# Kernel optimization log

Measured on AMD Instinct MI355X. Metric: run time of the kernel, lower is better.

The kernel has to match this reference:

```python
import jax, jax.numpy as jnp
import numpy as np

N_NODES = 8192
K = 64


def setup_inputs() -> dict:
    key = jax.random.key(0)
    k1, k2 = jax.random.split(key)
    A = jax.random.normal(k1, (N_NODES, N_NODES), dtype=jnp.float32)
    idx = jax.random.randint(k2, (N_NODES,), 0, N_NODES, dtype=jnp.int64)
    return {"A": A, "idx": idx}


def reference(A, idx):
    # adj = relu(A)
    adj = jax.nn.relu(A)
    # per-row top-k indices (dim=1), then scatter a 0/1 mask and multiply
    _, ind = jax.lax.top_k(adj, K)  # ind: [N, K]
    rows = jnp.arange(adj.shape[0], dtype=ind.dtype)[:, None]  # [N, 1]
    mask = jnp.zeros_like(adj).at[rows, ind].set(1.0)
    return adj * mask
```

## Files before the change

kernel.cpp:

```cpp
#include <hip/hip_runtime.h>
#include <stdint.h>


constexpr int N     = 8192;
constexpr int K     = 64;
constexpr int BLOCK = 256;
constexpr int VPT   = N / BLOCK;
constexpr int V4    = VPT / 4;
constexpr int EQ_CAP = 256;

__global__ __launch_bounds__(BLOCK) void topk_row_kernel(
    const float* __restrict__ A, float* __restrict__ out)
{
    __shared__ uint32_t hist[4][256];
    __shared__ uint32_t s_prefix;
    __shared__ uint32_t s_k;
    __shared__ uint32_t s_cnt;
    __shared__ int      s_tzero;
    __shared__ uint32_t s_eq[EQ_CAP];

    const int tid  = threadIdx.x;
    const int wave = tid >> 6;
    const int lane = tid & 63;
    const int row  = blockIdx.x;

    const float4* rowp = reinterpret_cast<const float4*>(A + (size_t)row * N);
    float4*       outp = reinterpret_cast<float4*>(out + (size_t)row * N);

    uint32_t v[VPT];
    #pragma unroll
    for (int j = 0; j < V4; ++j) {
        float4 f = rowp[tid + j * BLOCK];
        v[4*j+0] = (f.x > 0.f) ? __float_as_uint(f.x) : 0u;
        v[4*j+1] = (f.y > 0.f) ? __float_as_uint(f.y) : 0u;
        v[4*j+2] = (f.z > 0.f) ? __float_as_uint(f.z) : 0u;
        v[4*j+3] = (f.w > 0.f) ? __float_as_uint(f.w) : 0u;
    }

    #pragma unroll
    for (int j = 0; j < 4; ++j) hist[j][tid] = 0;
    if (tid == 0) { s_prefix = 0; s_k = K; s_cnt = 0; s_tzero = 0; }
    __syncthreads();

    #pragma unroll
    for (int j = 0; j < VPT; ++j) {
        uint32_t x = v[j];
        if (x) atomicAdd(&hist[wave][x >> 24], 1u);
    }
    __syncthreads();
    {
        uint32_t tot = hist[0][tid] + hist[1][tid] + hist[2][tid] + hist[3][tid];
        hist[0][tid] = tot;
    }
    __syncthreads();

    if (wave == 0) {
        uint32_t k  = s_k;
        uint32_t h0 = hist[0][4*lane+0];
        uint32_t h1 = hist[0][4*lane+1];
        uint32_t h2 = hist[0][4*lane+2];
        uint32_t h3 = hist[0][4*lane+3];
        uint32_t suf = h0 + h1 + h2 + h3;
        #pragma unroll
        for (int d = 1; d < 64; d <<= 1) {
            uint32_t o = __shfl_down(suf, d, 64);
            if (lane + d < 64) suf += o;
        }
        unsigned long long m = __ballot(suf >= k);
        if (m == 0ull) {
            if (lane == 0) s_tzero = 1;
        } else {
            int cl = 63 - __builtin_clzll(m);
            if (lane == cl) {
                uint32_t S0 = suf;
                uint32_t S1 = S0 - h0;
                uint32_t S2 = S1 - h1;
                uint32_t S3 = S2 - h2;
                int b; uint32_t Sb, hb;
                if      (S3 >= k) { b = 4*lane+3; Sb = S3; hb = h3; }
                else if (S2 >= k) { b = 4*lane+2; Sb = S2; hb = h2; }
                else if (S1 >= k) { b = 4*lane+1; Sb = S1; hb = h1; }
                else              { b = 4*lane+0; Sb = S0; hb = h0; }
                s_prefix |= (uint32_t)b << 24;
                s_k = k - (Sb - hb);
            }
        }
    }
    __syncthreads();

    if (s_tzero) {
        #pragma unroll
        for (int j = 0; j < V4; ++j) {
            float4 o;
            o.x = __uint_as_float(v[4*j+0]);
            o.y = __uint_as_float(v[4*j+1]);
            o.z = __uint_as_float(v[4*j+2]);
            o.w = __uint_as_float(v[4*j+3]);
            outp[tid + j * BLOCK] = o;
        }
        return;
    }

    for (int shift = 16; shift >= 0; shift -= 8) {
        uint32_t prefix = s_prefix;
        #pragma unroll
        for (int j = 0; j < 4; ++j) hist[j][tid] = 0;
        __syncthreads();

        const uint32_t himask = 0xFFFFFFFFu << (shift + 8);
        #pragma unroll
        for (int j = 0; j < VPT; ++j) {
            uint32_t x = v[j];
            if ((x & himask) == prefix)
                atomicAdd(&hist[wave][(x >> shift) & 255u], 1u);
        }
        __syncthreads();
        {
            uint32_t tot = hist[0][tid] + hist[1][tid] + hist[2][tid] + hist[3][tid];
            hist[0][tid] = tot;
        }
        __syncthreads();

        if (wave == 0) {
            uint32_t k  = s_k;
            uint32_t h0 = hist[0][4*lane+0];
            uint32_t h1 = hist[0][4*lane+1];
            uint32_t h2 = hist[0][4*lane+2];
            uint32_t h3 = hist[0][4*lane+3];
            uint32_t suf = h0 + h1 + h2 + h3;
            #pragma unroll
            for (int d = 1; d < 64; d <<= 1) {
                uint32_t o = __shfl_down(suf, d, 64);
                if (lane + d < 64) suf += o;
            }
            unsigned long long m = __ballot(suf >= k);
            int cl = 63 - __builtin_clzll(m);
            if (lane == cl) {
                uint32_t S0 = suf;
                uint32_t S1 = S0 - h0;
                uint32_t S2 = S1 - h1;
                uint32_t S3 = S2 - h2;
                int b; uint32_t Sb, hb;
                if      (S3 >= k) { b = 4*lane+3; Sb = S3; hb = h3; }
                else if (S2 >= k) { b = 4*lane+2; Sb = S2; hb = h2; }
                else if (S1 >= k) { b = 4*lane+1; Sb = S1; hb = h1; }
                else              { b = 4*lane+0; Sb = S0; hb = h0; }
                s_prefix |= (uint32_t)b << shift;
                s_k = k - (Sb - hb);
            }
        }
        __syncthreads();
    }

    const uint32_t T    = s_prefix;
    const uint32_t need = s_k;
    const float    Tf   = __uint_as_float(T);

    #pragma unroll
    for (int j = 0; j < V4; ++j) {
        const int base = (tid + j * BLOCK) * 4;
        float4 o;
        float* oc = &o.x;
        #pragma unroll
        for (int c = 0; c < 4; ++c) {
            uint32_t x = v[4*j+c];
            float val = 0.f;
            if (x > T) {
                val = __uint_as_float(x);
            } else if (x == T) {
                uint32_t p = atomicAdd(&s_cnt, 1u);
                if (p < EQ_CAP) s_eq[p] = (uint32_t)(base + c);
            }
            oc[c] = val;
        }
        outp[tid + j * BLOCK] = o;
    }
    __syncthreads();

    if (tid == 0) {
        uint32_t cnt = s_cnt < (uint32_t)EQ_CAP ? s_cnt : (uint32_t)EQ_CAP;
        for (uint32_t n = 0; n < need; ++n) {
            uint32_t best = 0xFFFFFFFFu, bi = 0;
            for (uint32_t i = 0; i < cnt; ++i) {
                if (s_eq[i] < best) { best = s_eq[i]; bi = i; }
            }
            if (best != 0xFFFFFFFFu) {
                s_eq[bi] = 0xFFFFFFFFu;
                out[(size_t)row * N + best] = Tf;
            }
        }
    }
}

extern "C" void kernel_launch(void* const* d_in, const int* in_sizes, int n_in,
                              void* d_out, int out_size, void* d_ws, size_t ws_size,
                              hipStream_t stream) {
    const float* A = (const float*)d_in[0];
    float* out = (float*)d_out;
    topk_row_kernel<<<N, BLOCK, 0, stream>>>(A, out);
}
```

Measured before the change: 445.3 us.

## Prefilter top-k candidates by exponent window into shared list before radix select

Computes the row max and counts positives in the top few exponent bins using register counters and wave reductions, picking an exponent cutoff that keeps at least K candidates. The candidates are compacted into a shared-memory list, and the four radix-select histogram passes then run only over that short list instead of all 8192 values per row. This is meant to cut the LDS atomic traffic of the per-pass histograms. It adds an extra max reduction, more barriers, about 6KB more shared memory, and a fallback to the full radix path when the candidate count exceeds the cap.

Result: no change. 442.9 us (-0.5%).

```diff
diff --git a/kernel.cpp b/kernel.cpp
--- a/kernel.cpp
+++ b/kernel.cpp
@@ -2,22 +2,57 @@
 #include <stdint.h>
 
 
-constexpr int N     = 8192;
-constexpr int K     = 64;
-constexpr int BLOCK = 256;
-constexpr int VPT   = N / BLOCK;
-constexpr int V4    = VPT / 4;
+constexpr int N      = 8192;
+constexpr int K      = 64;
+constexpr int BLOCK  = 256;
+constexpr int VPT    = N / BLOCK;
+constexpr int V4     = VPT / 4;
+constexpr int CAP    = 1536;
 constexpr int EQ_CAP = 256;
+
+__device__ __forceinline__ uint32_t wave_reduce_add(uint32_t x) {
+    #pragma unroll
+    for (int d = 32; d >= 1; d >>= 1) x += __shfl_down(x, d, 64);
+    return x;
+}
+
+__device__ __forceinline__ void scan_pick(const uint32_t* hist256,
+                                          uint32_t* s_prefix, uint32_t* s_k,
+                                          int shift, int lane) {
+    uint32_t k  = *s_k;
+    uint32_t h0 = hist256[4 * lane + 0];
+    uint32_t h1 = hist256[4 * lane + 1];
+    uint32_t h2 = hist256[4 * lane + 2];
+    uint32_t h3 = hist256[4 * lane + 3];
+    uint32_t suf = h0 + h1 + h2 + h3;
+    #pragma unroll
+    for (int d = 1; d < 64; d <<= 1) {
+        uint32_t o = __shfl_down(suf, d, 64);
+        if (lane + d < 64) suf += o;
+    }
+    unsigned long long m = __ballot(suf >= k);
+    int cl = 63 - __builtin_clzll(m);
+    if (lane == cl) {
+        uint32_t S0 = suf, S1 = S0 - h0, S2 = S1 - h1, S3 = S2 - h2;
+        int b; uint32_t Sb, hb;
+        if      (S3 >= k) { b = 3; Sb = S3; hb = h3; }
+        else if (S2 >= k) { b = 2; Sb = S2; hb = h2; }
+        else if (S1 >= k) { b = 1; Sb = S1; hb = h1; }
+        else              { b = 0; Sb = S0; hb = h0; }
+        *s_prefix |= (uint32_t)(4 * lane + b) << shift;
+        *s_k = k - (Sb - hb);
+    }
+}
 
 __global__ __launch_bounds__(BLOCK) void topk_row_kernel(
     const float* __restrict__ A, float* __restrict__ out)
 {
     __shared__ uint32_t hist[4][256];
-    __shared__ uint32_t s_prefix;
-    __shared__ uint32_t s_k;
-    __shared__ uint32_t s_cnt;
-    __shared__ int      s_tzero;
+    __shared__ uint32_t list[CAP];
     __shared__ uint32_t s_eq[EQ_CAP];
+    __shared__ uint32_t s_rb[4][5];
+    __shared__ uint32_t s_rmax[4];
+    __shared__ uint32_t s_prefix, s_k, s_cnt, s_listcnt, s_C, s_ecut, s_mode, s_max;
 
     const int tid  = threadIdx.x;
     const int wave = tid >> 6;
@@ -36,120 +71,189 @@
         v[4*j+2] = (f.z > 0.f) ? __float_as_uint(f.z) : 0u;
         v[4*j+3] = (f.w > 0.f) ? __float_as_uint(f.w) : 0u;
     }
-
-    #pragma unroll
-    for (int j = 0; j < 4; ++j) hist[j][tid] = 0;
-    if (tid == 0) { s_prefix = 0; s_k = K; s_cnt = 0; s_tzero = 0; }
-    __syncthreads();
-
+    if (tid == 0) { s_listcnt = 0; s_cnt = 0; }
+
+    uint32_t mx = 0;
+    #pragma unroll
+    for (int j = 0; j < VPT; ++j) mx = (v[j] > mx) ? v[j] : mx;
+    #pragma unroll
+    for (int d = 32; d >= 1; d >>= 1) {
+        uint32_t o = __shfl_down(mx, d, 64);
+        mx = (o > mx) ? o : mx;
+    }
+    if (lane == 0) s_rmax[wave] = mx;
+    __syncthreads();
+    if (tid == 0) {
+        uint32_t m = s_rmax[0];
+        m = (s_rmax[1] > m) ? s_rmax[1] : m;
+        m = (s_rmax[2] > m) ? s_rmax[2] : m;
+        m = (s_rmax[3] > m) ? s_rmax[3] : m;
+        s_max = m;
+    }
+    __syncthreads();
+    const uint32_t expM = s_max >> 23;
+
+    uint32_t b0 = 0, b1 = 0, b2 = 0, b3 = 0, cpos = 0;
     #pragma unroll
     for (int j = 0; j < VPT; ++j) {
         uint32_t x = v[j];
-        if (x) atomicAdd(&hist[wave][x >> 24], 1u);
-    }
-    __syncthreads();
-    {
-        uint32_t tot = hist[0][tid] + hist[1][tid] + hist[2][tid] + hist[3][tid];
-        hist[0][tid] = tot;
-    }
-    __syncthreads();
-
-    if (wave == 0) {
-        uint32_t k  = s_k;
-        uint32_t h0 = hist[0][4*lane+0];
-        uint32_t h1 = hist[0][4*lane+1];
-        uint32_t h2 = hist[0][4*lane+2];
-        uint32_t h3 = hist[0][4*lane+3];
-        uint32_t suf = h0 + h1 + h2 + h3;
-        #pragma unroll
-        for (int d = 1; d < 64; d <<= 1) {
-            uint32_t o = __shfl_down(suf, d, 64);
-            if (lane + d < 64) suf += o;
-        }
-        unsigned long long m = __ballot(suf >= k);
-        if (m == 0ull) {
-            if (lane == 0) s_tzero = 1;
+        if (x != 0u) {
+            uint32_t d = expM - (x >> 23);
+            cpos += 1u;
+            b0 += (d == 0u); b1 += (d == 1u); b2 += (d == 2u); b3 += (d == 3u);
+        }
+    }
+    b0 = wave_reduce_add(b0); b1 = wave_reduce_add(b1);
+    b2 = wave_reduce_add(b2); b3 = wave_reduce_add(b3);
+    cpos = wave_reduce_add(cpos);
+    if (lane == 0) {
+        s_rb[wave][0] = b0; s_rb[wave][1] = b1; s_rb[wave][2] = b2;
+        s_rb[wave][3] = b3; s_rb[wave][4] = cpos;
+    }
+    __syncthreads();
+    if (tid == 0) {
+        uint32_t B[5];
+        #pragma unroll
+        for (int c = 0; c < 5; ++c)
+            B[c] = s_rb[0][c] + s_rb[1][c] + s_rb[2][c] + s_rb[3][c];
+        if (B[4] < (uint32_t)K) {
+            s_mode = 1;
         } else {
-            int cl = 63 - __builtin_clzll(m);
-            if (lane == cl) {
-                uint32_t S0 = suf;
-                uint32_t S1 = S0 - h0;
-                uint32_t S2 = S1 - h1;
-                uint32_t S3 = S2 - h2;
-                int b; uint32_t Sb, hb;
-                if      (S3 >= k) { b = 4*lane+3; Sb = S3; hb = h3; }
-                else if (S2 >= k) { b = 4*lane+2; Sb = S2; hb = h2; }
-                else if (S1 >= k) { b = 4*lane+1; Sb = S1; hb = h1; }
-                else              { b = 4*lane+0; Sb = S0; hb = h0; }
-                s_prefix |= (uint32_t)b << 24;
-                s_k = k - (Sb - hb);
-            }
-        }
-    }
-    __syncthreads();
-
-    if (s_tzero) {
+            s_mode = 0;
+            uint32_t cum = 0; int jf = -1;
+            #pragma unroll
+            for (int j = 0; j < 4; ++j) {
+                cum += B[j];
+                if (jf < 0 && cum >= (uint32_t)K) jf = j;
+            }
+            if (jf >= 0) {
+                uint32_t c2 = 0;
+                for (int j = 0; j <= jf; ++j) c2 += B[j];
+                s_C = c2; s_ecut = expM - (uint32_t)jf;
+            } else {
+                s_C = 0;
+            }
+        }
+    }
+    __syncthreads();
+
+    if (s_mode == 1) {
         #pragma unroll
         for (int j = 0; j < V4; ++j) {
             float4 o;
-            o.x = __uint_as_float(v[4*j+0]);
-            o.y = __uint_as_float(v[4*j+1]);
-            o.z = __uint_as_float(v[4*j+2]);
-            o.w = __uint_as_float(v[4*j+3]);
+            o.x = __uint_as_float(v[4*j+0]); o.y = __uint_as_float(v[4*j+1]);
+            o.z = __uint_as_float(v[4*j+2]); o.w = __uint_as_float(v[4*j+3]);
             outp[tid + j * BLOCK] = o;
         }
         return;
     }
 
-    for (int shift = 16; shift >= 0; shift -= 8) {
-        uint32_t prefix = s_prefix;
-        #pragma unroll
-        for (int j = 0; j < 4; ++j) hist[j][tid] = 0;
-        __syncthreads();
-
-        const uint32_t himask = 0xFFFFFFFFu << (shift + 8);
+    if (s_C == 0) {
+        uint32_t ecut = (expM > 7u) ? (expM - 7u) : 0u;
+        for (;;) {
+            __syncthreads();
+            uint32_t lc = 0;
+            #pragma unroll
+            for (int j = 0; j < VPT; ++j)
+                lc += (v[j] != 0u && (v[j] >> 23) >= ecut) ? 1u : 0u;
+            lc = wave_reduce_add(lc);
+            if (lane == 0) s_rb[wave][0] = lc;
+            __syncthreads();
+            if (tid == 0) {
+                s_C = s_rb[0][0] + s_rb[1][0] + s_rb[2][0] + s_rb[3][0];
+                s_ecut = ecut;
+            }
+            __syncthreads();
+            if (s_C >= (uint32_t)K || ecut == 0u) break;
+            ecut = (ecut > 4u) ? (ecut - 4u) : 0u;
+        }
+    }
+    __syncthreads();
+    const uint32_t C    = s_C;
+    const uint32_t ecut = s_ecut;
+
+    #pragma unroll
+    for (int c = 0; c < 4; ++c) hist[c][tid] = 0;
+    if (tid == 0) { s_prefix = 0; s_k = K; }
+    __syncthreads();
+
+    if (C <= (uint32_t)CAP) {
+        uint32_t lc = 0;
+        #pragma unroll
+        for (int j = 0; j < VPT; ++j)
+            lc += (v[j] != 0u && (v[j] >> 23) >= ecut) ? 1u : 0u;
+        uint32_t incl = lc;
+        #pragma unroll
+        for (int d = 1; d < 64; d <<= 1) {
+            uint32_t t = __shfl_up(incl, d, 64);
+            if (lane >= d) incl += t;
+        }
+        uint32_t baseV = 0;
+        if (lane == 63) baseV = atomicAdd(&s_listcnt, incl);
+        uint32_t base = __shfl(baseV, 63, 64);
+        uint32_t pos  = base + (incl - lc);
         #pragma unroll
         for (int j = 0; j < VPT; ++j) {
             uint32_t x = v[j];
-            if ((x & himask) == prefix)
-                atomicAdd(&hist[wave][(x >> shift) & 255u], 1u);
-        }
-        __syncthreads();
-        {
-            uint32_t tot = hist[0][tid] + hist[1][tid] + hist[2][tid] + hist[3][tid];
-            hist[0][tid] = tot;
-        }
-        __syncthreads();
-
-        if (wave == 0) {
-            uint32_t k  = s_k;
-            uint32_t h0 = hist[0][4*lane+0];
-            uint32_t h1 = hist[0][4*lane+1];
-            uint32_t h2 = hist[0][4*lane+2];
-            uint32_t h3 = hist[0][4*lane+3];
-            uint32_t suf = h0 + h1 + h2 + h3;
-            #pragma unroll
-            for (int d = 1; d < 64; d <<= 1) {
-                uint32_t o = __shfl_down(suf, d, 64);
-                if (lane + d < 64) suf += o;
-            }
-            unsigned long long m = __ballot(suf >= k);
-            int cl = 63 - __builtin_clzll(m);
-            if (lane == cl) {
-                uint32_t S0 = suf;
-                uint32_t S1 = S0 - h0;
-                uint32_t S2 = S1 - h1;
-                uint32_t S3 = S2 - h2;
-                int b; uint32_t Sb, hb;
-                if      (S3 >= k) { b = 4*lane+3; Sb = S3; hb = h3; }
-                else if (S2 >= k) { b = 4*lane+2; Sb = S2; hb = h2; }
-                else if (S1 >= k) { b = 4*lane+1; Sb = S1; hb = h1; }
-                else              { b = 4*lane+0; Sb = S0; hb = h0; }
-                s_prefix |= (uint32_t)b << shift;
-                s_k = k - (Sb - hb);
-            }
-        }
-        __syncthreads();
+            if (x != 0u && (x >> 23) >= ecut) list[pos++] = x;
+        }
+        __syncthreads();
+
+        for (uint32_t i = tid; i < C; i += BLOCK)
+            atomicAdd(&hist[wave][list[i] >> 24], 1u);
+        __syncthreads();
+        hist[0][tid] = hist[0][tid] + hist[1][tid] + hist[2][tid] + hist[3][tid];
+        __syncthreads();
+        if (wave == 0) scan_pick(hist[0], &s_prefix, &s_k, 24, lane);
+        __syncthreads();
+
+        for (int shift = 16; shift >= 0; shift -= 8) {
+            const uint32_t prefix = s_prefix;
+            #pragma unroll
+            for (int c = 0; c < 4; ++c) hist[c][tid] = 0;
+            __syncthreads();
+            const uint32_t himask = 0xFFFFFFFFu << (shift + 8);
+            for (uint32_t i = tid; i < C; i += BLOCK) {
+                uint32_t x = list[i];
+                if ((x & himask) == prefix)
+                    atomicAdd(&hist[wave][(x >> shift) & 255u], 1u);
+            }
+            __syncthreads();
+            hist[0][tid] = hist[0][tid] + hist[1][tid] + hist[2][tid] + hist[3][tid];
+            __syncthreads();
+            if (wave == 0) scan_pick(hist[0], &s_prefix, &s_k, shift, lane);
+            __syncthreads();
+        }
+    } else {
+        #pragma unroll
+        for (int j = 0; j < VPT; ++j) {
+            uint32_t x = v[j];
+            if (x) atomicAdd(&hist[wave][x >> 24], 1u);
+        }
+        __syncthreads();
+        hist[0][tid] = hist[0][tid] + hist[1][tid] + hist[2][tid] + hist[3][tid];
+        __syncthreads();
+        if (wave == 0) scan_pick(hist[0], &s_prefix, &s_k, 24, lane);
+        __syncthreads();
+
+        for (int shift = 16; shift >= 0; shift -= 8) {
+            const uint32_t prefix = s_prefix;
+            #pragma unroll
+            for (int c = 0; c < 4; ++c) hist[c][tid] = 0;
+            __syncthreads();
+            const uint32_t himask = 0xFFFFFFFFu << (shift + 8);
+            #pragma unroll
+            for (int j = 0; j < VPT; ++j) {
+                uint32_t x = v[j];
+                if ((x & himask) == prefix)
+                    atomicAdd(&hist[wave][(x >> shift) & 255u], 1u);
+            }
+            __syncthreads();
+            hist[0][tid] = hist[0][tid] + hist[1][tid] + hist[2][tid] + hist[3][tid];
+            __syncthreads();
+            if (wave == 0) scan_pick(hist[0], &s_prefix, &s_k, shift, lane);
+            __syncthreads();
+        }
     }
 
     const uint32_t T    = s_prefix;
@@ -169,7 +273,7 @@
                 val = __uint_as_float(x);
             } else if (x == T) {
                 uint32_t p = atomicAdd(&s_cnt, 1u);
-                if (p < EQ_CAP) s_eq[p] = (uint32_t)(base + c);
+                if (p < (uint32_t)EQ_CAP) s_eq[p] = (uint32_t)(base + c);
             }
             oc[c] = val;
         }
@@ -181,9 +285,8 @@
         uint32_t cnt = s_cnt < (uint32_t)EQ_CAP ? s_cnt : (uint32_t)EQ_CAP;
         for (uint32_t n = 0; n < need; ++n) {
             uint32_t best = 0xFFFFFFFFu, bi = 0;
-            for (uint32_t i = 0; i < cnt; ++i) {
+            for (uint32_t i = 0; i < cnt; ++i)
                 if (s_eq[i] < best) { best = s_eq[i]; bi = i; }
-            }
             if (best != 0xFFFFFFFFu) {
                 s_eq[bi] = 0xFFFFFFFFu;
                 out[(size_t)row * N + best] = Tf;
```
